# Kernel tuning notes

Hardware: AMD Instinct MI355X
Metric: run time of the kernel (lower is better)

Reference implementation:

```python
import jax, jax.numpy as jnp
import numpy as np

B, S, D = 8, 2048, 1024


def setup_inputs() -> dict:
    key = jax.random.key(0)
    k1, k2, k3, k4 = jax.random.split(key, 4)
    scale = 1.0 / np.sqrt(D)
    x = jax.random.normal(k1, (B, S, D), dtype=jnp.float32)
    Wq = jax.random.normal(k2, (D, D), dtype=jnp.float32) * scale
    Wk = jax.random.normal(k3, (D, D), dtype=jnp.float32) * scale
    Wv = jax.random.normal(k4, (D, D), dtype=jnp.float32) * scale
    return {"x": x, "Wq": Wq, "Wk": Wk, "Wv": Wv}


def reference(x, Wq, Wk, Wv):
    # nn.Linear(d, d, bias=False): y = x @ W.T
    q = jnp.einsum('bsd,ed->bse', x, Wq)
    k = jnp.einsum('bsd,ed->bse', x, Wk)
    v = jnp.einsum('bsd,ed->bse', x, Wv)
    S_len = x.shape[1]
    d_k = k.shape[-1]
    # full score matrix, causal mask (strict upper triangle -> -inf)
    scores = jnp.einsum('bqd,bkd->bqk', q, k)
    causal = jnp.triu(jnp.ones((S_len, S_len), dtype=bool), k=1)
    scores = jnp.where(causal[None, :, :], -jnp.inf, scores)
    attn = jax.nn.softmax(scores / jnp.sqrt(jnp.asarray(d_k, scores.dtype)), axis=-1)
    # dropout p=0.0 (eval) -> identity
    return jnp.einsum('bqk,bkd->bqd', attn, v)
```

## Files before the change

### kernel.cpp

```cpp
#include <hip/hip_runtime.h>


typedef _Float16 v8h __attribute__((ext_vector_type(8)));
typedef _Float16 v4h __attribute__((ext_vector_type(4)));
typedef float    v4f __attribute__((ext_vector_type(4)));

#define TM 128
#define TN 128
#define BK 64

__device__ __forceinline__ void async16(const _Float16* g, _Float16* l) {
  __builtin_amdgcn_global_load_lds(
      (__attribute__((address_space(1))) void*)(void*)g,
      (__attribute__((address_space(3))) void*)l, 16, 0, 0);
}

__device__ __forceinline__ void stage_tile(const _Float16* Ag, int lda,
                                           const _Float16* Bg, int ldb,
                                           _Float16* As, _Float16* Bs,
                                           int w, int lane) {
#pragma unroll
  for (int r = 0; r < 4; ++r) {
    const int c = w * 256 + r * 64 + lane;
    const int row = c >> 3;
    const int sc = (c & 7) ^ (row & 7);
    async16(Ag + (size_t)row * lda + sc * 8, As + (w * 256 + r * 64) * 8);
    async16(Bg + (size_t)row * ldb + sc * 8, Bs + (w * 256 + r * 64) * 8);
  }
}

__device__ __forceinline__ void mfma_slab(const _Float16* As, const _Float16* Bs,
                                          int wr, int wc, int lr, int quad,
                                          v4f acc[4][4]) {
#pragma unroll
  for (int ks = 0; ks < 2; ++ks) {
    v8h a[4], b[4];
#pragma unroll
    for (int i = 0; i < 4; ++i) {
      const int ra = wr + i * 16 + lr;
      const int rb = wc + i * 16 + lr;
      a[i] = *(const v8h*)&As[ra * BK + (((ks * 4 + quad) ^ (ra & 7)) * 8)];
      b[i] = *(const v8h*)&Bs[rb * BK + (((ks * 4 + quad) ^ (rb & 7)) * 8)];
    }
#pragma unroll
    for (int i = 0; i < 4; ++i)
#pragma unroll
      for (int j = 0; j < 4; ++j)
        acc[i][j] = __builtin_amdgcn_mfma_f32_16x16x32_f16(a[i], b[j],
                                                           acc[i][j], 0, 0, 0);
  }
}

#define PIPE_STEP(STAGE_NEXT, HAVE_NEXT)                                     \
  do {                                                                       \
    if (HAVE_NEXT) {                                                         \
      STAGE_NEXT;                                                            \
      asm volatile("s_waitcnt vmcnt(8)" ::: "memory");                       \
    } else {                                                                 \
      asm volatile("s_waitcnt vmcnt(0)" ::: "memory");                       \
    }                                                                        \
    __builtin_amdgcn_s_barrier();                                            \
    __builtin_amdgcn_sched_barrier(0);                                       \
    __builtin_amdgcn_s_setprio(1);                                           \
    mfma_slab(As[cur], Bs[cur], wr, wc, lr, quad, acc);                      \
    __builtin_amdgcn_s_setprio(0);                                           \
    __builtin_amdgcn_sched_barrier(0);                                       \
    __builtin_amdgcn_s_barrier();                                            \
  } while (0)

__device__ __forceinline__ void grid_swz(int& bx, int& by) {
  const int gx = gridDim.x;
  const int n = gx * gridDim.y;
  const int f = blockIdx.x + blockIdx.y * gx;
  const int s = (f & 7) * (n >> 3) + (f >> 3);
  bx = s % gx;
  by = s / gx;
}

__global__ __launch_bounds__(256)
void cvt_f16(const float* __restrict__ src, _Float16* __restrict__ dst) {
  const int i = (blockIdx.x * 256 + threadIdx.x) * 8;
  float4 a = *(const float4*)(src + i);
  float4 b = *(const float4*)(src + i + 4);
  v8h o = {(_Float16)a.x, (_Float16)a.y, (_Float16)a.z, (_Float16)a.w,
           (_Float16)b.x, (_Float16)b.y, (_Float16)b.z, (_Float16)b.w};
  *(v8h*)(dst + i) = o;
}

__global__ __launch_bounds__(256)
void proj_gemm(const _Float16* __restrict__ X, const _Float16* __restrict__ W,
               _Float16* __restrict__ Qb, _Float16* __restrict__ Kb,
               _Float16* __restrict__ Vt) {
  const int tid = threadIdx.x;
  int bx, by;
  grid_swz(bx, by);
  const int n0 = bx * TN, m0 = by * TM;
  const int which = n0 >> 10;
  const int nw = n0 & 1023;

  __shared__ _Float16 As[2][TM * BK];
  __shared__ _Float16 Bs[2][TN * BK];

  const int lane = tid & 63, w = tid >> 6;
  const int wr = (w >> 1) * 64, wc = (w & 1) * 64;
  const int lr = lane & 15, quad = lane >> 4;

  v4f acc[4][4];
#pragma unroll
  for (int i = 0; i < 4; ++i)
#pragma unroll
    for (int j = 0; j < 4; ++j) acc[i][j] = (v4f){0.f, 0.f, 0.f, 0.f};

  const _Float16* Ab = X + (size_t)m0 * 1024;
  const _Float16* Bb = W + (size_t)n0 * 1024;
  const int NK = 1024 / BK;

  stage_tile(Ab, 1024, Bb, 1024, As[0], Bs[0], w, lane);
  for (int kt = 0; kt < NK; ++kt) {
    const int cur = kt & 1;
    PIPE_STEP(stage_tile(Ab + (kt + 1) * BK, 1024, Bb + (kt + 1) * BK, 1024,
                         As[cur ^ 1], Bs[cur ^ 1], w, lane),
              kt + 1 < NK);
  }

#pragma unroll
  for (int i = 0; i < 4; ++i) {
    const int r0 = m0 + wr + i * 16 + quad * 4;
#pragma unroll
    for (int j = 0; j < 4; ++j) {
      const int cl = wc + j * 16 + lr;
      if (which < 2) {
        _Float16* dst = (which == 0) ? Qb : Kb;
        const int col = nw + cl;
#pragma unroll
        for (int rg = 0; rg < 4; ++rg)
          dst[(size_t)(r0 + rg) * 1024 + col] = (_Float16)acc[i][j][rg];
      } else {
        const int d = nw + cl;
        const int b = r0 >> 11, s = r0 & 2047;
        v4h o = {(_Float16)acc[i][j][0], (_Float16)acc[i][j][1],
                 (_Float16)acc[i][j][2], (_Float16)acc[i][j][3]};
        *(v4h*)(Vt + (size_t)b * 1024 * 2048 + (size_t)d * 2048 + s) = o;
      }
    }
  }
}

__global__ __launch_bounds__(256)
void scores_gemm(const _Float16* __restrict__ Q, const _Float16* __restrict__ K,
                 _Float16* __restrict__ Sc) {
  const int tid = threadIdx.x;
  int bx, by;
  grid_swz(bx, by);
  const int bz = blockIdx.z;
  const int n0 = bx * TN, m0 = by * TM;
  _Float16* Cb = Sc + (size_t)bz * 2048 * 2048;

  if (bx > by) {
    const _Float16 ninf = (_Float16)(-__builtin_inff());
    v8h mv = {ninf, ninf, ninf, ninf, ninf, ninf, ninf, ninf};
#pragma unroll
    for (int it = 0; it < 8; ++it) {
      int ch = it * 256 + tid;
      int r = ch >> 4, cc = (ch & 15) * 8;
      *(v8h*)(Cb + (size_t)(m0 + r) * 2048 + n0 + cc) = mv;
    }
    return;
  }

  __shared__ _Float16 As[2][TM * BK];
  __shared__ _Float16 Bs[2][TN * BK];
  const _Float16* Qb = Q + (size_t)bz * 2048 * 1024;
  const _Float16* Kb = K + (size_t)bz * 2048 * 1024;

  const int lane = tid & 63, w = tid >> 6;
  const int wr = (w >> 1) * 64, wc = (w & 1) * 64;
  const int lr = lane & 15, quad = lane >> 4;

  v4f acc[4][4];
#pragma unroll
  for (int i = 0; i < 4; ++i)
#pragma unroll
    for (int j = 0; j < 4; ++j) acc[i][j] = (v4f){0.f, 0.f, 0.f, 0.f};

  const _Float16* Ab = Qb + (size_t)m0 * 1024;
  const _Float16* Bb = Kb + (size_t)n0 * 1024;
  const int NK = 1024 / BK;

  stage_tile(Ab, 1024, Bb, 1024, As[0], Bs[0], w, lane);
  for (int kt = 0; kt < NK; ++kt) {
    const int cur = kt & 1;
    PIPE_STEP(stage_tile(Ab + (kt + 1) * BK, 1024, Bb + (kt + 1) * BK, 1024,
                         As[cur ^ 1], Bs[cur ^ 1], w, lane),
              kt + 1 < NK);
  }

  const _Float16 ninf = (_Float16)(-__builtin_inff());
#pragma unroll
  for (int i = 0; i < 4; ++i) {
    const int r0 = m0 + wr + i * 16 + quad * 4;
#pragma unroll
    for (int j = 0; j < 4; ++j) {
      const int cc = n0 + wc + j * 16 + lr;
#pragma unroll
      for (int rg = 0; rg < 4; ++rg) {
        const int rr = r0 + rg;
        Cb[(size_t)rr * 2048 + cc] = (cc > rr) ? ninf : (_Float16)acc[i][j][rg];
      }
    }
  }
}

__global__ __launch_bounds__(256)
void softmax_rows(_Float16* __restrict__ Sc) {
  _Float16* base = Sc + (size_t)blockIdx.x * 2048;
  const int tid = threadIdx.x;
  const int lane = tid & 63, w = tid >> 6;

  v8h pv = *(const v8h*)(base + tid * 8);
  float f[8];
#pragma unroll
  for (int j = 0; j < 8; ++j) f[j] = (float)pv[j];

  float mx = f[0];
#pragma unroll
  for (int j = 1; j < 8; ++j) mx = fmaxf(mx, f[j]);
#pragma unroll
  for (int off = 32; off; off >>= 1) mx = fmaxf(mx, __shfl_xor(mx, off));
  __shared__ float redm[4], reds[4];
  if (lane == 0) redm[w] = mx;
  __syncthreads();
  mx = fmaxf(fmaxf(redm[0], redm[1]), fmaxf(redm[2], redm[3]));

  const float scale = 0.03125f;
  float e[8], s = 0.f;
#pragma unroll
  for (int j = 0; j < 8; ++j) {
    e[j] = __expf((f[j] - mx) * scale);
    s += e[j];
  }
#pragma unroll
  for (int off = 32; off; off >>= 1) s += __shfl_xor(s, off);
  if (lane == 0) reds[w] = s;
  __syncthreads();
  s = reds[0] + reds[1] + reds[2] + reds[3];
  const float inv = 1.0f / s;
#pragma unroll
  for (int j = 0; j < 8; ++j) pv[j] = (_Float16)(e[j] * inv);
  *(v8h*)(base + tid * 8) = pv;
}

__global__ __launch_bounds__(256)
void pv_gemm(const _Float16* __restrict__ P, const _Float16* __restrict__ Vt,
             float* __restrict__ Out) {
  const int tid = threadIdx.x;
  int bx, by;
  grid_swz(bx, by);
  const int bz = blockIdx.z;
  const int n0 = bx * TN, m0 = by * TM;
  const _Float16* Pb = P + (size_t)bz * 2048 * 2048;
  const _Float16* Vb = Vt + (size_t)bz * 1024 * 2048;
  float* Cb = Out + (size_t)bz * 2048 * 1024;

  __shared__ _Float16 As[2][TM * BK];
  __shared__ _Float16 Bs[2][TN * BK];

  const int lane = tid & 63, w = tid >> 6;
  const int wr = (w >> 1) * 64, wc = (w & 1) * 64;
  const int lr = lane & 15, quad = lane >> 4;

  v4f acc[4][4];
#pragma unroll
  for (int i = 0; i < 4; ++i)
#pragma unroll
    for (int j = 0; j < 4; ++j) acc[i][j] = (v4f){0.f, 0.f, 0.f, 0.f};

  const _Float16* Ab = Pb + (size_t)m0 * 2048;
  const _Float16* Bb = Vb + (size_t)n0 * 2048;
  const int NK = (by + 1) * 2;

  stage_tile(Ab, 2048, Bb, 2048, As[0], Bs[0], w, lane);
  for (int kt = 0; kt < NK; ++kt) {
    const int cur = kt & 1;
    PIPE_STEP(stage_tile(Ab + (kt + 1) * BK, 2048, Bb + (kt + 1) * BK, 2048,
                         As[cur ^ 1], Bs[cur ^ 1], w, lane),
              kt + 1 < NK);
  }

#pragma unroll
  for (int i = 0; i < 4; ++i) {
    const int r0 = m0 + wr + i * 16 + quad * 4;
#pragma unroll
    for (int j = 0; j < 4; ++j) {
      const int cc = n0 + wc + j * 16 + lr;
#pragma unroll
      for (int rg = 0; rg < 4; ++rg)
        Cb[(size_t)(r0 + rg) * 1024 + cc] = acc[i][j][rg];
    }
  }
}

extern "C" void kernel_launch(void* const* d_in, const int* in_sizes, int n_in,
                              void* d_out, int out_size, void* d_ws, size_t ws_size,
                              hipStream_t stream) {
  const int B = 8, S = 2048, D = 1024;
  const int M = B * S;
  const float* x  = (const float*)d_in[0];
  const float* Wq = (const float*)d_in[1];
  const float* Wk = (const float*)d_in[2];
  const float* Wv = (const float*)d_in[3];
  float* out = (float*)d_out;

  char* ws = (char*)d_ws;
  _Float16* Qb = (_Float16*)ws;
  _Float16* Kb = (_Float16*)(ws + (size_t)33554432);
  _Float16* Vt = (_Float16*)(ws + (size_t)67108864);
  _Float16* Sc = (_Float16*)(ws + (size_t)100663296);
  _Float16* xh = Sc;
  _Float16* Wh = Sc + (size_t)M * D;

  cvt_f16<<<(M * D) / 2048, 256, 0, stream>>>(x, xh);
  cvt_f16<<<(D * D) / 2048, 256, 0, stream>>>(Wq, Wh);
  cvt_f16<<<(D * D) / 2048, 256, 0, stream>>>(Wk, Wh + (size_t)D * D);
  cvt_f16<<<(D * D) / 2048, 256, 0, stream>>>(Wv, Wh + (size_t)2 * D * D);

  proj_gemm<<<dim3(24, M / TM, 1), 256, 0, stream>>>(xh, Wh, Qb, Kb, Vt);

  scores_gemm<<<dim3(S / TN, S / TM, B), 256, 0, stream>>>(Qb, Kb, Sc);

  softmax_rows<<<B * S, 256, 0, stream>>>(Sc);

  pv_gemm<<<dim3(D / TN, S / TM, B), 256, 0, stream>>>(Sc, Vt, out);
}
```

Baseline: 456.0 us.

## Enlarge GEMM tiles to 256x256 with 512 threads and deeper split-K pipeline

```diff
diff --git a/kernel.cpp b/kernel.cpp
--- a/kernel.cpp
+++ b/kernel.cpp
@@ -5,8 +5,8 @@
 typedef _Float16 v4h __attribute__((ext_vector_type(4)));
 typedef float    v4f __attribute__((ext_vector_type(4)));
 
-#define TM 128
-#define TN 128
+#define BM 256
+#define BN 256
 #define BK 64
 
 __device__ __forceinline__ void async16(const _Float16* g, _Float16* l) {
@@ -15,58 +15,85 @@
       (__attribute__((address_space(3))) void*)l, 16, 0, 0);
 }
 
-__device__ __forceinline__ void stage_tile(const _Float16* Ag, int lda,
-                                           const _Float16* Bg, int ldb,
-                                           _Float16* As, _Float16* Bs,
+__device__ __forceinline__ void stage_pair(const _Float16* GA, int lda,
+                                           const _Float16* GB, int ldb,
+                                           _Float16* lds, int t, int ks,
                                            int w, int lane) {
-#pragma unroll
-  for (int r = 0; r < 4; ++r) {
-    const int c = w * 256 + r * 64 + lane;
-    const int row = c >> 3;
-    const int sc = (c & 7) ^ (row & 7);
-    async16(Ag + (size_t)row * lda + sc * 8, As + (w * 256 + r * 64) * 8);
-    async16(Bg + (size_t)row * ldb + sc * 8, Bs + (w * 256 + r * 64) * 8);
-  }
-}
-
-__device__ __forceinline__ void mfma_slab(const _Float16* As, const _Float16* Bs,
-                                          int wr, int wc, int lr, int quad,
-                                          v4f acc[4][4]) {
-#pragma unroll
-  for (int ks = 0; ks < 2; ++ks) {
-    v8h a[4], b[4];
-#pragma unroll
-    for (int i = 0; i < 4; ++i) {
-      const int ra = wr + i * 16 + lr;
-      const int rb = wc + i * 16 + lr;
-      a[i] = *(const v8h*)&As[ra * BK + (((ks * 4 + quad) ^ (ra & 7)) * 8)];
-      b[i] = *(const v8h*)&Bs[rb * BK + (((ks * 4 + quad) ^ (rb & 7)) * 8)];
-    }
-#pragma unroll
-    for (int i = 0; i < 4; ++i)
-#pragma unroll
-      for (int j = 0; j < 4; ++j)
-        acc[i][j] = __builtin_amdgcn_mfma_f32_16x16x32_f16(a[i], b[j],
-                                                           acc[i][j], 0, 0, 0);
-  }
-}
-
-#define PIPE_STEP(STAGE_NEXT, HAVE_NEXT)                                     \
+  _Float16* UA = lds + ((size_t)((t & 1) * 2 + ks)) * 8192;
+  _Float16* UB = lds + 32768 + ((size_t)((t & 1) * 2 + ks)) * 8192;
+  const _Float16* ga = GA + t * 64 + ks * 32;
+  const _Float16* gb = GB + t * 64 + ks * 32;
+#pragma unroll
+  for (int g = 0; g < 2; ++g) {
+    const int cb = g * 512 + w * 64;
+    const int c = cb + lane;
+    const int row = c & 255, col8 = c >> 8;
+    async16(ga + (size_t)row * lda + col8 * 8, UA + cb * 8);
+    async16(gb + (size_t)row * ldb + col8 * 8, UB + cb * 8);
+  }
+}
+
+__device__ __forceinline__ void mfma_phase(const _Float16* UA, const _Float16* UB,
+                                           int wr, int wc, int lr, int quad,
+                                           v4f acc[8][4]) {
+  v8h a[8], b[4];
+#pragma unroll
+  for (int i = 0; i < 8; ++i)
+    a[i] = *(const v8h*)&UA[(quad * 256 + wr + i * 16 + lr) * 8];
+#pragma unroll
+  for (int j = 0; j < 4; ++j)
+    b[j] = *(const v8h*)&UB[(quad * 256 + wc + j * 16 + lr) * 8];
+  __builtin_amdgcn_s_setprio(1);
+#pragma unroll
+  for (int i = 0; i < 8; ++i)
+#pragma unroll
+    for (int j = 0; j < 4; ++j)
+      acc[i][j] = __builtin_amdgcn_mfma_f32_16x16x32_f16(a[i], b[j],
+                                                         acc[i][j], 0, 0, 0);
+  __builtin_amdgcn_s_setprio(0);
+}
+
+__device__ __forceinline__ void gemm_loop(const _Float16* Ab, int lda,
+                                          const _Float16* Bb, int ldb,
+                                          int NK, _Float16* lds,
+                                          int w, int lane, int wr, int wc,
+                                          int lr, int quad, v4f acc[8][4]) {
+  stage_pair(Ab, lda, Bb, ldb, lds, 0, 0, w, lane);
+  stage_pair(Ab, lda, Bb, ldb, lds, 0, 1, w, lane);
+  stage_pair(Ab, lda, Bb, ldb, lds, 1, 0, w, lane);
+
+#define PH(KS, SLOT, DOSTAGE, ST, SKS, VM)                                   \
   do {                                                                       \
-    if (HAVE_NEXT) {                                                         \
-      STAGE_NEXT;                                                            \
-      asm volatile("s_waitcnt vmcnt(8)" ::: "memory");                       \
-    } else {                                                                 \
-      asm volatile("s_waitcnt vmcnt(0)" ::: "memory");                       \
-    }                                                                        \
+    if (DOSTAGE) stage_pair(Ab, lda, Bb, ldb, lds, ST, SKS, w, lane);        \
+    asm volatile("s_waitcnt vmcnt(" #VM ")" ::: "memory");                   \
+    asm volatile("" ::: "memory");                                           \
     __builtin_amdgcn_s_barrier();                                            \
-    __builtin_amdgcn_sched_barrier(0);                                       \
-    __builtin_amdgcn_s_setprio(1);                                           \
-    mfma_slab(As[cur], Bs[cur], wr, wc, lr, quad, acc);                      \
-    __builtin_amdgcn_s_setprio(0);                                           \
-    __builtin_amdgcn_sched_barrier(0);                                       \
+    asm volatile("" ::: "memory");                                           \
+    mfma_phase(lds + ((size_t)((SLOT) * 2 + (KS))) * 8192,                   \
+               lds + 32768 + ((size_t)((SLOT) * 2 + (KS))) * 8192,           \
+               wr, wc, lr, quad, acc);                                       \
+    asm volatile("" ::: "memory");                                           \
     __builtin_amdgcn_s_barrier();                                            \
+    asm volatile("" ::: "memory");                                           \
   } while (0)
+
+  for (int kt = 0; kt < NK - 2; ++kt) {
+    const int sl = kt & 1;
+    PH(0, sl, true, kt + 1, 1, 12);
+    PH(1, sl, true, kt + 2, 0, 12);
+  }
+  {
+    const int kt = NK - 2, sl = kt & 1;
+    PH(0, sl, true, kt + 1, 1, 12);
+    PH(1, sl, false, 0, 0, 8);
+  }
+  {
+    const int kt = NK - 1, sl = kt & 1;
+    PH(0, sl, false, 0, 0, 4);
+    PH(1, sl, false, 0, 0, 0);
+  }
+#undef PH
+}
 
 __device__ __forceinline__ void grid_swz(int& bx, int& by) {
   const int gx = gridDim.x;
@@ -87,44 +114,33 @@
   *(v8h*)(dst + i) = o;
 }
 
-__global__ __launch_bounds__(256)
+__global__ __launch_bounds__(512, 2)
 void proj_gemm(const _Float16* __restrict__ X, const _Float16* __restrict__ W,
                _Float16* __restrict__ Qb, _Float16* __restrict__ Kb,
                _Float16* __restrict__ Vt) {
+  __shared__ _Float16 lds[65536];
   const int tid = threadIdx.x;
   int bx, by;
   grid_swz(bx, by);
-  const int n0 = bx * TN, m0 = by * TM;
+  const int n0 = bx * BN, m0 = by * BM;
   const int which = n0 >> 10;
   const int nw = n0 & 1023;
 
-  __shared__ _Float16 As[2][TM * BK];
-  __shared__ _Float16 Bs[2][TN * BK];
-
   const int lane = tid & 63, w = tid >> 6;
-  const int wr = (w >> 1) * 64, wc = (w & 1) * 64;
+  const int wr = (w >> 2) * 128, wc = (w & 3) * 64;
   const int lr = lane & 15, quad = lane >> 4;
 
-  v4f acc[4][4];
-#pragma unroll
-  for (int i = 0; i < 4; ++i)
+  v4f acc[8][4];
+#pragma unroll
+  for (int i = 0; i < 8; ++i)
 #pragma unroll
     for (int j = 0; j < 4; ++j) acc[i][j] = (v4f){0.f, 0.f, 0.f, 0.f};
 
-  const _Float16* Ab = X + (size_t)m0 * 1024;
-  const _Float16* Bb = W + (size_t)n0 * 1024;
-  const int NK = 1024 / BK;
-
-  stage_tile(Ab, 1024, Bb, 1024, As[0], Bs[0], w, lane);
-  for (int kt = 0; kt < NK; ++kt) {
-    const int cur = kt & 1;
-    PIPE_STEP(stage_tile(Ab + (kt + 1) * BK, 1024, Bb + (kt + 1) * BK, 1024,
-                         As[cur ^ 1], Bs[cur ^ 1], w, lane),
-              kt + 1 < NK);
-  }
-
-#pragma unroll
-  for (int i = 0; i < 4; ++i) {
+  gemm_loop(X + (size_t)m0 * 1024, 1024, W + (size_t)n0 * 1024, 1024,
+            1024 / BK, lds, w, lane, wr, wc, lr, quad, acc);
+
+#pragma unroll
+  for (int i = 0; i < 8; ++i) {
     const int r0 = m0 + wr + i * 16 + quad * 4;
 #pragma unroll
     for (int j = 0; j < 4; ++j) {
@@ -146,58 +162,48 @@
   }
 }
 
-__global__ __launch_bounds__(256)
+__global__ __launch_bounds__(512, 2)
 void scores_gemm(const _Float16* __restrict__ Q, const _Float16* __restrict__ K,
                  _Float16* __restrict__ Sc) {
+  __shared__ _Float16 lds[65536];
   const int tid = threadIdx.x;
   int bx, by;
   grid_swz(bx, by);
   const int bz = blockIdx.z;
-  const int n0 = bx * TN, m0 = by * TM;
+  const int n0 = bx * BN, m0 = by * BM;
   _Float16* Cb = Sc + (size_t)bz * 2048 * 2048;
 
   if (bx > by) {
     const _Float16 ninf = (_Float16)(-__builtin_inff());
     v8h mv = {ninf, ninf, ninf, ninf, ninf, ninf, ninf, ninf};
 #pragma unroll
-    for (int it = 0; it < 8; ++it) {
-      int ch = it * 256 + tid;
-      int r = ch >> 4, cc = (ch & 15) * 8;
+    for (int it = 0; it < 16; ++it) {
+      int ch = it * 512 + tid;
+      int r = ch >> 5, cc = (ch & 31) * 8;
       *(v8h*)(Cb + (size_t)(m0 + r) * 2048 + n0 + cc) = mv;
     }
     return;
   }
 
-  __shared__ _Float16 As[2][TM * BK];
-  __shared__ _Float16 Bs[2][TN * BK];
-  const _Float16* Qb = Q + (size_t)bz * 2048 * 1024;
-  const _Float16* Kb = K + (size_t)bz * 2048 * 1024;
+  const _Float16* Qz = Q + (size_t)bz * 2048 * 1024;
+  const _Float16* Kz = K + (size_t)bz * 2048 * 1024;
 
   const int lane = tid & 63, w = tid >> 6;
-  const int wr = (w >> 1) * 64, wc = (w & 1) * 64;
+  const int wr = (w >> 2) * 128, wc = (w & 3) * 64;
   const int lr = lane & 15, quad = lane >> 4;
 
-  v4f acc[4][4];
-#pragma unroll
-  for (int i = 0; i < 4; ++i)
+  v4f acc[8][4];
+#pragma unroll
+  for (int i = 0; i < 8; ++i)
 #pragma unroll
     for (int j = 0; j < 4; ++j) acc[i][j] = (v4f){0.f, 0.f, 0.f, 0.f};
 
-  const _Float16* Ab = Qb + (size_t)m0 * 1024;
-  const _Float16* Bb = Kb + (size_t)n0 * 1024;
-  const int NK = 1024 / BK;
-
-  stage_tile(Ab, 1024, Bb, 1024, As[0], Bs[0], w, lane);
-  for (int kt = 0; kt < NK; ++kt) {
-    const int cur = kt & 1;
-    PIPE_STEP(stage_tile(Ab + (kt + 1) * BK, 1024, Bb + (kt + 1) * BK, 1024,
-                         As[cur ^ 1], Bs[cur ^ 1], w, lane),
-              kt + 1 < NK);
-  }
+  gemm_loop(Qz + (size_t)m0 * 1024, 1024, Kz + (size_t)n0 * 1024, 1024,
+            1024 / BK, lds, w, lane, wr, wc, lr, quad, acc);
 
   const _Float16 ninf = (_Float16)(-__builtin_inff());
 #pragma unroll
-  for (int i = 0; i < 4; ++i) {
+  for (int i = 0; i < 8; ++i) {
     const int r0 = m0 + wr + i * 16 + quad * 4;
 #pragma unroll
     for (int j = 0; j < 4; ++j) {
@@ -250,45 +256,34 @@
   *(v8h*)(base + tid * 8) = pv;
 }
 
-__global__ __launch_bounds__(256)
+__global__ __launch_bounds__(512, 2)
 void pv_gemm(const _Float16* __restrict__ P, const _Float16* __restrict__ Vt,
              float* __restrict__ Out) {
+  __shared__ _Float16 lds[65536];
   const int tid = threadIdx.x;
   int bx, by;
   grid_swz(bx, by);
   const int bz = blockIdx.z;
-  const int n0 = bx * TN, m0 = by * TM;
+  const int n0 = bx * BN, m0 = by * BM;
   const _Float16* Pb = P + (size_t)bz * 2048 * 2048;
   const _Float16* Vb = Vt + (size_t)bz * 1024 * 2048;
   float* Cb = Out + (size_t)bz * 2048 * 1024;
 
-  __shared__ _Float16 As[2][TM * BK];
-  __shared__ _Float16 Bs[2][TN * BK];
-
   const int lane = tid & 63, w = tid >> 6;
-  const int wr = (w >> 1) * 64, wc = (w & 1) * 64;
+  const int wr = (w >> 2) * 128, wc = (w & 3) * 64;
   const int lr = lane & 15, quad = lane >> 4;
 
-  v4f acc[4][4];
-#pragma unroll
-  for (int i = 0; i < 4; ++i)
+  v4f acc[8][4];
+#pragma unroll
+  for (int i = 0; i < 8; ++i)
 #pragma unroll
     for (int j = 0; j < 4; ++j) acc[i][j] = (v4f){0.f, 0.f, 0.f, 0.f};
 
-  const _Float16* Ab = Pb + (size_t)m0 * 2048;
-  const _Float16* Bb = Vb + (size_t)n0 * 2048;
-  const int NK = (by + 1) * 2;
-
-  stage_tile(Ab, 2048, Bb, 2048, As[0], Bs[0], w, lane);
-  for (int kt = 0; kt < NK; ++kt) {
-    const int cur = kt & 1;
-    PIPE_STEP(stage_tile(Ab + (kt + 1) * BK, 2048, Bb + (kt + 1) * BK, 2048,
-                         As[cur ^ 1], Bs[cur ^ 1], w, lane),
-              kt + 1 < NK);
-  }
-
-#pragma unroll
-  for (int i = 0; i < 4; ++i) {
+  gemm_loop(Pb + (size_t)m0 * 2048, 2048, Vb + (size_t)n0 * 2048, 2048,
+            (by + 1) * 4, lds, w, lane, wr, wc, lr, quad, acc);
+
+#pragma unroll
+  for (int i = 0; i < 8; ++i) {
     const int r0 = m0 + wr + i * 16 + quad * 4;
 #pragma unroll
     for (int j = 0; j < 4; ++j) {
@@ -324,11 +319,11 @@
   cvt_f16<<<(D * D) / 2048, 256, 0, stream>>>(Wk, Wh + (size_t)D * D);
   cvt_f16<<<(D * D) / 2048, 256, 0, stream>>>(Wv, Wh + (size_t)2 * D * D);
 
-  proj_gemm<<<dim3(24, M / TM, 1), 256, 0, stream>>>(xh, Wh, Qb, Kb, Vt);
-
-  scores_gemm<<<dim3(S / TN, S / TM, B), 256, 0, stream>>>(Qb, Kb, Sc);
+  proj_gemm<<<dim3(12, M / BM, 1), 512, 0, stream>>>(xh, Wh, Qb, Kb, Vt);
+
+  scores_gemm<<<dim3(S / BN, S / BM, B), 512, 0, stream>>>(Qb, Kb, Sc);
 
   softmax_rows<<<B * S, 256, 0, stream>>>(Sc);
 
-  pv_gemm<<<dim3(D / TN, S / TM, B), 256, 0, stream>>>(Sc, Vt, out);
-}
+  pv_gemm<<<dim3(D / BN, S / BM, B), 512, 0, stream>>>(Sc, Vt, out);
+}
```

After: 574.2 us. 25.9% more time.
